# Kernel tuning notes

Measured on AMD Instinct MI355X. Metric: run time of the kernel, lower is better.

Reference implementation:

```python
import jax, jax.numpy as jnp
import numpy as np

B, N, D_IN, D_OUT = 2, 4096, 768, 768


def setup_inputs() -> dict:
    key = jax.random.key(0)
    kx, kq, kk, kv = jax.random.split(key, 4)
    x = jax.random.normal(kx, (B, N, D_IN), dtype=jnp.float32)
    # Linear(d_in, d_out, bias=False) weights, stored as [d_in, d_out]
    scale = 1.0 / np.sqrt(D_IN)
    Wq = jax.random.normal(kq, (D_IN, D_OUT), dtype=jnp.float32) * scale
    Wk = jax.random.normal(kk, (D_IN, D_OUT), dtype=jnp.float32) * scale
    Wv = jax.random.normal(kv, (D_IN, D_OUT), dtype=jnp.float32) * scale
    return {"x": x, "Wq": Wq, "Wk": Wk, "Wv": Wv}


def reference(x, Wq, Wk, Wv):
    # q,k,v: [B, N, D_OUT]
    q = jnp.einsum('bnd,de->bne', x, Wq)
    k = jnp.einsum('bnd,de->bne', x, Wk)
    v = jnp.einsum('bnd,de->bne', x, Wv)
    # Full [B, N, N] score matrix (naive attention, as in source).
    # NOTE: source's masked_fill is non-in-place and discarded, so NO causal
    # mask is actually applied -- reproduced faithfully here.
    scores = jnp.einsum('bqe,bke->bqk', q, k) / jnp.sqrt(jnp.float32(k.shape[-1]))
    weights = jax.nn.softmax(scores, axis=-1)
    # dropout rate 0.0 / eval mode -> identity
    out = jnp.einsum('bqk,bke->bqe', weights, v)  # [B, N, D_OUT]
    return out
```

## Files before the change

kernel.cpp:

```cpp
#include <hip/hip_runtime.h>

typedef __bf16 bf16x8 __attribute__((ext_vector_type(8)));
typedef float f32x4 __attribute__((ext_vector_type(4)));
typedef unsigned short us8 __attribute__((ext_vector_type(8)));

#define GAS __attribute__((address_space(1)))
#define LAS __attribute__((address_space(3)))

__device__ __forceinline__ unsigned short f32_to_bf16(float f) {
    unsigned int u = __float_as_uint(f);
    u += 0x7FFFu + ((u >> 16) & 1u);
    return (unsigned short)(u >> 16);
}

__device__ __forceinline__ float bf16_to_f32(unsigned short h) {
    return __uint_as_float((unsigned int)h << 16);
}

__device__ __forceinline__ void load16(const unsigned short* g, unsigned short* l) {
    __builtin_amdgcn_global_load_lds((GAS unsigned int*)g, (LAS unsigned int*)l, 16, 0, 0);
}

__global__ __launch_bounds__(1024) void prep(
    const float* __restrict__ x, unsigned short* __restrict__ Xbf,
    const float* __restrict__ W0, const float* __restrict__ W1, const float* __restrict__ W2,
    unsigned short* __restrict__ T0, unsigned short* __restrict__ T1, unsigned short* __restrict__ T2)
{
    __shared__ float tile[32][33];
    const int id = blockIdx.x;
    const int t = threadIdx.x;
    if (id < 1536) {
        int i = id * 1024 + t;
        float4 v = ((const float4*)x)[i];
        ushort4 o;
        o.x = f32_to_bf16(v.x); o.y = f32_to_bf16(v.y);
        o.z = f32_to_bf16(v.z); o.w = f32_to_bf16(v.w);
        ((ushort4*)Xbf)[i] = o;
    } else {
        const int tid = id - 1536;
        const int z = tid / 576, rem = tid % 576;
        const int by = rem / 24, bx = rem % 24;
        const float* W = (z == 0) ? W0 : (z == 1) ? W1 : W2;
        unsigned short* T = (z == 0) ? T0 : (z == 1) ? T1 : T2;
        const int r0 = by * 32, c0 = bx * 32;
        const int tx = t & 31, ty = t >> 5;
        tile[ty][tx] = W[(size_t)(r0 + ty) * 768 + c0 + tx];
        __syncthreads();
        T[(size_t)(c0 + ty) * 768 + r0 + tx] = f32_to_bf16(tile[tx][ty]);
    }
}

template <typename CT>
__global__ __launch_bounds__(256) void gemm_nt(
    const unsigned short* __restrict__ A, const unsigned short* __restrict__ B,
    CT* __restrict__ C, int K, int lda, int ldb, int ldc,
    size_t sA, size_t sB, size_t sC, float alpha)
{
    A += (size_t)blockIdx.z * sA;
    B += (size_t)blockIdx.z * sB;
    C += (size_t)blockIdx.z * sC;
    const int m0 = blockIdx.y * 128;
    const int n0 = blockIdx.x * 128;
    const int t = threadIdx.x;
    const int lane = t & 63;
    const int w = t >> 6;
    const int wm = (w >> 1) * 64;
    const int wn = (w & 1) * 64;

    __shared__ unsigned short At[128 * 64];
    __shared__ unsigned short Bt[128 * 64];

    f32x4 acc[4][4];
#pragma unroll
    for (int i = 0; i < 4; ++i)
#pragma unroll
        for (int j = 0; j < 4; ++j) acc[i][j] = (f32x4){0.f, 0.f, 0.f, 0.f};

    const int r15 = lane & 15;
    const int qa = lane >> 4;

    for (int k0 = 0; k0 < K; k0 += 64) {
#pragma unroll
        for (int i = 0; i < 4; ++i) {
            const int c = i * 256 + t;
            const int row = c >> 3;
            const int cc = (c & 7) ^ (row & 7);
            load16(A + (size_t)(m0 + row) * lda + k0 + cc * 8, &At[c * 8]);
            load16(B + (size_t)(n0 + row) * ldb + k0 + cc * 8, &Bt[c * 8]);
        }
        __syncthreads();

#pragma unroll
        for (int ks = 0; ks < 2; ++ks) {
            bf16x8 af[4], bf[4];
#pragma unroll
            for (int mi = 0; mi < 4; ++mi) {
                const int row = wm + mi * 16 + r15;
                af[mi] = *(const bf16x8*)&At[row * 64 + (((ks << 2) + qa) ^ (row & 7)) * 8];
            }
#pragma unroll
            for (int ni = 0; ni < 4; ++ni) {
                const int row = wn + ni * 16 + r15;
                bf[ni] = *(const bf16x8*)&Bt[row * 64 + (((ks << 2) + qa) ^ (row & 7)) * 8];
            }
#pragma unroll
            for (int mi = 0; mi < 4; ++mi)
#pragma unroll
                for (int ni = 0; ni < 4; ++ni)
                    acc[mi][ni] = __builtin_amdgcn_mfma_f32_16x16x32_bf16(
                        af[mi], bf[ni], acc[mi][ni], 0, 0, 0);
        }
        __syncthreads();
    }

    const int cr = (lane >> 4) * 4;
#pragma unroll
    for (int mi = 0; mi < 4; ++mi) {
#pragma unroll
        for (int ni = 0; ni < 4; ++ni) {
            const int gm = m0 + wm + mi * 16 + cr;
            const int gn = n0 + wn + ni * 16 + r15;
#pragma unroll
            for (int r = 0; r < 4; ++r) {
                float v = alpha * acc[mi][ni][r];
                if constexpr (sizeof(CT) == 2)
                    C[(size_t)(gm + r) * ldc + gn] = (CT)f32_to_bf16(v);
                else
                    C[(size_t)(gm + r) * ldc + gn] = v;
            }
        }
    }
}

template <int NT, bool EXP>
__device__ __forceinline__ void gemm256_core(
    const unsigned short* __restrict__ A, const unsigned short* __restrict__ B,
    unsigned short* __restrict__ C,
    int m0, int n0, int lda, int ldb, int ldc, float alpha)
{
    __shared__ unsigned short As[2][256 * 64];
    __shared__ unsigned short Bs[2][256 * 64];

    const int t = threadIdx.x;
    const int lane = t & 63;
    const int w = t >> 6;
    const int wm = (w >> 2) * 128;
    const int wn = (w & 3) * 64;
    const int r15 = lane & 15;
    const int qa = lane >> 4;

    const unsigned short* srcA[4];
    const unsigned short* srcB[4];
    int dstOff[4];
#pragma unroll
    for (int i = 0; i < 4; ++i) {
        const int c = i * 512 + t;
        const int row = c >> 3;
        const int cc = (c & 7) ^ (row & 7);
        srcA[i] = A + (size_t)(m0 + row) * lda + cc * 8;
        srcB[i] = B + (size_t)(n0 + row) * ldb + cc * 8;
        dstOff[i] = c * 8;
    }

    auto stageA = [&](int b, int kbase) {
#pragma unroll
        for (int i = 0; i < 4; ++i)
            load16(srcA[i] + kbase, &As[b][dstOff[i]]);
    };
    auto stageB = [&](int b, int kbase) {
#pragma unroll
        for (int i = 0; i < 4; ++i)
            load16(srcB[i] + kbase, &Bs[b][dstOff[i]]);
    };

    int offA[8][2], offB[4][2];
#pragma unroll
    for (int mi = 0; mi < 8; ++mi) {
        const int row = wm + mi * 16 + r15;
#pragma unroll
        for (int ks = 0; ks < 2; ++ks)
            offA[mi][ks] = row * 64 + (((ks << 2) + qa) ^ (row & 7)) * 8;
    }
#pragma unroll
    for (int ni = 0; ni < 4; ++ni) {
        const int row = wn + ni * 16 + r15;
#pragma unroll
        for (int ks = 0; ks < 2; ++ks)
            offB[ni][ks] = row * 64 + (((ks << 2) + qa) ^ (row & 7)) * 8;
    }

    f32x4 acc[8][4];
#pragma unroll
    for (int i = 0; i < 8; ++i)
#pragma unroll
        for (int j = 0; j < 4; ++j) acc[i][j] = (f32x4){0.f, 0.f, 0.f, 0.f};

    stageA(0, 0);
    stageB(0, 0);
    asm volatile("s_waitcnt vmcnt(0)" ::: "memory");
    __builtin_amdgcn_s_barrier();

    for (int tt = 0; tt < NT; ++tt) {
        const int b = tt & 1;
        const bool st = (tt + 1) < NT;
        const int kn = (tt + 1) << 6;

#pragma unroll
        for (int ks = 0; ks < 2; ++ks) {
            bf16x8 bB[4];
#pragma unroll
            for (int mh = 0; mh < 2; ++mh) {
                bf16x8 aA[4];
#pragma unroll
                for (int i = 0; i < 4; ++i)
                    aA[i] = *(const bf16x8*)&As[b][offA[mh * 4 + i][ks]];
                if (mh == 0) {
#pragma unroll
                    for (int ni = 0; ni < 4; ++ni)
                        bB[ni] = *(const bf16x8*)&Bs[b][offB[ni][ks]];
                }
                if (ks == 0 && mh == 0 && st) {
                    stageA(b ^ 1, kn);
                    stageB(b ^ 1, kn);
                }

                __builtin_amdgcn_s_barrier();
                asm volatile("s_waitcnt lgkmcnt(0)" ::: "memory");
                __builtin_amdgcn_s_setprio(1);
#pragma unroll
                for (int i = 0; i < 4; ++i)
#pragma unroll
                    for (int ni = 0; ni < 4; ++ni)
                        acc[mh * 4 + i][ni] = __builtin_amdgcn_mfma_f32_16x16x32_bf16(
                            aA[i], bB[ni], acc[mh * 4 + i][ni], 0, 0, 0);
                __builtin_amdgcn_s_setprio(0);
                if (ks == 1 && mh == 1) {
                    asm volatile("s_waitcnt vmcnt(0)" ::: "memory");
                    __builtin_amdgcn_s_barrier();
                } else {
                    __builtin_amdgcn_s_barrier();
                }
            }
        }
    }

    const int cr = (lane >> 4) * 4;
#pragma unroll
    for (int mi = 0; mi < 8; ++mi) {
#pragma unroll
        for (int ni = 0; ni < 4; ++ni) {
            const int gm = m0 + wm + mi * 16 + cr;
            const int gn = n0 + wn + ni * 16 + r15;
#pragma unroll
            for (int r = 0; r < 4; ++r) {
                float v = alpha * acc[mi][ni][r];
                if constexpr (EXP) v = __expf(v);
                C[(size_t)(gm + r) * ldc + gn] = f32_to_bf16(v);
            }
        }
    }
}

__global__ __launch_bounds__(512, 2) void gemm_s_exp2(
    const unsigned short* __restrict__ Q, const unsigned short* __restrict__ Kb,
    unsigned short* __restrict__ Sexp, float alpha)
{
    const unsigned short* A = Q + (size_t)blockIdx.z * 3145728;
    const unsigned short* B = Kb + (size_t)blockIdx.z * 3145728;
    unsigned short* C = Sexp + (size_t)blockIdx.z * 16777216;
    gemm256_core<12, true>(A, B, C, blockIdx.y * 256, blockIdx.x * 256,
                           768, 768, 4096, alpha);
}

__global__ __launch_bounds__(512, 2) void gemm_splitk2(
    const unsigned short* __restrict__ P, const unsigned short* __restrict__ Vt,
    unsigned short* __restrict__ Part)
{
    const int z = blockIdx.z;
    const int batch = z & 1;
    const int split = z >> 1;
    const unsigned short* A = P + (size_t)batch * 16777216 + (size_t)split * 2048;
    const unsigned short* B = Vt + (size_t)batch * 4096 + (size_t)split * 2048;
    unsigned short* C = Part + (size_t)z * 3145728;
    gemm256_core<32, false>(A, B, C, blockIdx.y * 256, blockIdx.x * 256,
                            4096, 8192, 768, 1.0f);
}

__global__ __launch_bounds__(256) void reduce_norm_rows(
    const unsigned short* __restrict__ Sexp, const unsigned short* __restrict__ Part,
    float* __restrict__ out)
{
    const int g = blockIdx.x;
    const int batch = g >> 12;
    const int r = g & 4095;
    const int t = threadIdx.x;
    const int wv = t >> 6, ln = t & 63;

    const unsigned short* srow = Sexp + (size_t)batch * 16777216 + (size_t)r * 4096;
    us8 a = ((const us8*)srow)[t];
    us8 b = ((const us8*)srow)[t + 256];
    float s = 0.f;
#pragma unroll
    for (int j = 0; j < 8; ++j) s += bf16_to_f32(a[j]) + bf16_to_f32(b[j]);
#pragma unroll
    for (int off = 32; off > 0; off >>= 1) s += __shfl_down(s, off, 64);
    __shared__ float red[4];
    if (ln == 0) red[wv] = s;
    __syncthreads();
    const float inv = 1.f / (red[0] + red[1] + red[2] + red[3]);

    if (t < 192) {
        const int c = t * 4;
        float4 acc = {0.f, 0.f, 0.f, 0.f};
#pragma unroll
        for (int sgroup = 0; sgroup < 2; ++sgroup) {
            const unsigned short* p = Part
                + ((size_t)(sgroup * 2 + batch) * 4096 + r) * 768 + c;
            ushort4 u = *(const ushort4*)p;
            acc.x += bf16_to_f32(u.x);
            acc.y += bf16_to_f32(u.y);
            acc.z += bf16_to_f32(u.z);
            acc.w += bf16_to_f32(u.w);
        }
        float4 o;
        o.x = acc.x * inv; o.y = acc.y * inv; o.z = acc.z * inv; o.w = acc.w * inv;
        *(float4*)(out + (size_t)g * 768 + c) = o;
    }
}

extern "C" void kernel_launch(void* const* d_in, const int* in_sizes, int n_in,
                              void* d_out, int out_size, void* d_ws, size_t ws_size,
                              hipStream_t stream) {
    const float* x  = (const float*)d_in[0];
    const float* Wq = (const float*)d_in[1];
    const float* Wk = (const float*)d_in[2];
    const float* Wv = (const float*)d_in[3];
    float* out = (float*)d_out;

    char* base = (char*)d_ws;
    size_t off = 0;
    auto alloc = [&](size_t b) { char* p = base + off; off += (b + 255) & ~(size_t)255; return p; };

    unsigned short* Xbf = (unsigned short*)alloc(8192ull * 768 * 2);
    unsigned short* WqT = (unsigned short*)alloc(768ull * 768 * 2);
    unsigned short* WkT = (unsigned short*)alloc(768ull * 768 * 2);
    unsigned short* WvT = (unsigned short*)alloc(768ull * 768 * 2);
    unsigned short* Qb  = (unsigned short*)alloc(8192ull * 768 * 2);
    unsigned short* Kb  = (unsigned short*)alloc(8192ull * 768 * 2);
    unsigned short* Vt  = (unsigned short*)alloc(768ull * 8192 * 2);
    unsigned short* Sexp = (unsigned short*)alloc(2ull * 4096 * 4096 * 2);
    unsigned short* Part = (unsigned short*)alloc(4ull * 3145728 * 2);
    (void)ws_size; (void)in_sizes; (void)n_in; (void)out_size; (void)WkT;

    prep<<<dim3(3264), dim3(1024), 0, stream>>>(x, Xbf, Wq, Wk, Wv, WqT, WkT, WvT);
    gemm_nt<unsigned short><<<dim3(6, 64, 2), dim3(256), 0, stream>>>(
        Xbf, WqT, Qb, 768, 768, 768, 768,
         0,  589824,  6291456, 1.0f);
    gemm_nt<unsigned short><<<dim3(64, 6, 1), dim3(256), 0, stream>>>(
        WvT, Xbf, Vt, 768, 768, 768, 8192, 0, 0, 0, 1.0f);
    gemm_s_exp2<<<dim3(16, 16, 2), dim3(512), 0, stream>>>(
        Qb, Kb, Sexp, 0.03608439182435161f);
    gemm_splitk2<<<dim3(3, 16, 4), dim3(512), 0, stream>>>(Sexp, Vt, Part);
    reduce_norm_rows<<<dim3(8192), dim3(256), 0, stream>>>(Sexp, Part, out);
}
```

Measured before the change: 275.9 us.

## Prefetch two K-tiles ahead, map blocks to XCDs, retile split-K GEMM to 256x192

The core GEMM now issues loads for the next two K-tiles up front and refills a buffer right after consuming it. It waits with partial vmcnt counts instead of draining all loads every iteration, so global-to-LDS copies overlap more compute. Both attention GEMMs use a 1D grid with an explicit block-to-XCD mapping so neighbouring tiles share an XCD's L2. The PV split-K GEMM switches to 256x192 tiles, giving 256 blocks instead of 192 to fill the CUs better. The hardcoded vmcnt values depend on load counts per stage and are fragile if the tile shape changes.

Result: no change. 270.5 us (-1.9%).

```diff
diff --git a/kernel.cpp b/kernel.cpp
--- a/kernel.cpp
+++ b/kernel.cpp
@@ -132,48 +132,55 @@
     }
 }
 
-template <int NT, bool EXP>
+template <int NT, int BN64, bool EXP>
 __device__ __forceinline__ void gemm256_core(
     const unsigned short* __restrict__ A, const unsigned short* __restrict__ B,
     unsigned short* __restrict__ C,
     int m0, int n0, int lda, int ldb, int ldc, float alpha)
 {
+    constexpr int BN = BN64 * 64;
     __shared__ unsigned short As[2][256 * 64];
-    __shared__ unsigned short Bs[2][256 * 64];
+    __shared__ unsigned short Bs[2][BN * 64];
 
     const int t = threadIdx.x;
     const int lane = t & 63;
     const int w = t >> 6;
     const int wm = (w >> 2) * 128;
-    const int wn = (w & 3) * 64;
+    const int wn = (w & 3) * (BN / 4);
     const int r15 = lane & 15;
     const int qa = lane >> 4;
 
     const unsigned short* srcA[4];
-    const unsigned short* srcB[4];
-    int dstOff[4];
+    int dstA[4];
 #pragma unroll
     for (int i = 0; i < 4; ++i) {
         const int c = i * 512 + t;
         const int row = c >> 3;
         const int cc = (c & 7) ^ (row & 7);
         srcA[i] = A + (size_t)(m0 + row) * lda + cc * 8;
+        dstA[i] = c * 8;
+    }
+    const unsigned short* srcB[BN64];
+    int dstB[BN64];
+#pragma unroll
+    for (int i = 0; i < BN64; ++i) {
+        const int c = i * 512 + t;
+        const int row = c >> 3;
+        const int cc = (c & 7) ^ (row & 7);
         srcB[i] = B + (size_t)(n0 + row) * ldb + cc * 8;
-        dstOff[i] = c * 8;
-    }
-
-    auto stageA = [&](int b, int kbase) {
+        dstB[i] = c * 8;
+    }
+
+    auto stage = [&](int buf, int kbase) {
 #pragma unroll
         for (int i = 0; i < 4; ++i)
-            load16(srcA[i] + kbase, &As[b][dstOff[i]]);
+            load16(srcA[i] + kbase, &As[buf][dstA[i]]);
+#pragma unroll
+        for (int i = 0; i < BN64; ++i)
+            load16(srcB[i] + kbase, &Bs[buf][dstB[i]]);
     };
-    auto stageB = [&](int b, int kbase) {
-#pragma unroll
-        for (int i = 0; i < 4; ++i)
-            load16(srcB[i] + kbase, &Bs[b][dstOff[i]]);
-    };
-
-    int offA[8][2], offB[4][2];
+
+    int offA[8][2], offB[BN64][2];
 #pragma unroll
     for (int mi = 0; mi < 8; ++mi) {
         const int row = wm + mi * 16 + r15;
@@ -182,32 +189,37 @@
             offA[mi][ks] = row * 64 + (((ks << 2) + qa) ^ (row & 7)) * 8;
     }
 #pragma unroll
-    for (int ni = 0; ni < 4; ++ni) {
+    for (int ni = 0; ni < BN64; ++ni) {
         const int row = wn + ni * 16 + r15;
 #pragma unroll
         for (int ks = 0; ks < 2; ++ks)
             offB[ni][ks] = row * 64 + (((ks << 2) + qa) ^ (row & 7)) * 8;
     }
 
-    f32x4 acc[8][4];
+    f32x4 acc[8][BN64];
 #pragma unroll
     for (int i = 0; i < 8; ++i)
 #pragma unroll
-        for (int j = 0; j < 4; ++j) acc[i][j] = (f32x4){0.f, 0.f, 0.f, 0.f};
-
-    stageA(0, 0);
-    stageB(0, 0);
-    asm volatile("s_waitcnt vmcnt(0)" ::: "memory");
-    __builtin_amdgcn_s_barrier();
+        for (int j = 0; j < BN64; ++j) acc[i][j] = (f32x4){0.f, 0.f, 0.f, 0.f};
+
+    stage(0, 0);
+    stage(1, 64);
 
     for (int tt = 0; tt < NT; ++tt) {
         const int b = tt & 1;
-        const bool st = (tt + 1) < NT;
-        const int kn = (tt + 1) << 6;
+
+        if (tt == NT - 1) {
+            asm volatile("s_waitcnt vmcnt(0)" ::: "memory");
+        } else if constexpr (BN64 == 4) {
+            asm volatile("s_waitcnt vmcnt(8)" ::: "memory");
+        } else {
+            asm volatile("s_waitcnt vmcnt(7)" ::: "memory");
+        }
+        __builtin_amdgcn_s_barrier();
 
 #pragma unroll
         for (int ks = 0; ks < 2; ++ks) {
-            bf16x8 bB[4];
+            bf16x8 bB[BN64];
 #pragma unroll
             for (int mh = 0; mh < 2; ++mh) {
                 bf16x8 aA[4];
@@ -216,12 +228,8 @@
                     aA[i] = *(const bf16x8*)&As[b][offA[mh * 4 + i][ks]];
                 if (mh == 0) {
 #pragma unroll
-                    for (int ni = 0; ni < 4; ++ni)
+                    for (int ni = 0; ni < BN64; ++ni)
                         bB[ni] = *(const bf16x8*)&Bs[b][offB[ni][ks]];
-                }
-                if (ks == 0 && mh == 0 && st) {
-                    stageA(b ^ 1, kn);
-                    stageB(b ^ 1, kn);
                 }
 
                 __builtin_amdgcn_s_barrier();
@@ -230,25 +238,22 @@
 #pragma unroll
                 for (int i = 0; i < 4; ++i)
 #pragma unroll
-                    for (int ni = 0; ni < 4; ++ni)
+                    for (int ni = 0; ni < BN64; ++ni)
                         acc[mh * 4 + i][ni] = __builtin_amdgcn_mfma_f32_16x16x32_bf16(
                             aA[i], bB[ni], acc[mh * 4 + i][ni], 0, 0, 0);
                 __builtin_amdgcn_s_setprio(0);
-                if (ks == 1 && mh == 1) {
-                    asm volatile("s_waitcnt vmcnt(0)" ::: "memory");
-                    __builtin_amdgcn_s_barrier();
-                } else {
-                    __builtin_amdgcn_s_barrier();
-                }
-            }
-        }
+                __builtin_amdgcn_s_barrier();
+            }
+        }
+
+        if (tt + 2 < NT) stage(b, (tt + 2) << 6);
     }
 
     const int cr = (lane >> 4) * 4;
 #pragma unroll
     for (int mi = 0; mi < 8; ++mi) {
 #pragma unroll
-        for (int ni = 0; ni < 4; ++ni) {
+        for (int ni = 0; ni < BN64; ++ni) {
             const int gm = m0 + wm + mi * 16 + cr;
             const int gn = n0 + wn + ni * 16 + r15;
 #pragma unroll
@@ -265,25 +270,34 @@
     const unsigned short* __restrict__ Q, const unsigned short* __restrict__ Kb,
     unsigned short* __restrict__ Sexp, float alpha)
 {
-    const unsigned short* A = Q + (size_t)blockIdx.z * 3145728;
-    const unsigned short* B = Kb + (size_t)blockIdx.z * 3145728;
-    unsigned short* C = Sexp + (size_t)blockIdx.z * 16777216;
-    gemm256_core<12, true>(A, B, C, blockIdx.y * 256, blockIdx.x * 256,
-                           768, 768, 4096, alpha);
+    const int f = blockIdx.x;
+    const int xcd = f & 7;
+    const int local = f >> 3;
+    const int x = (xcd & 1) * 8 + (local & 7);
+    const int y = ((xcd >> 1) & 1) * 8 + (local >> 3);
+    const int bb = xcd >> 2;
+    const unsigned short* A = Q + (size_t)bb * 3145728;
+    const unsigned short* B = Kb + (size_t)bb * 3145728;
+    unsigned short* C = Sexp + (size_t)bb * 16777216;
+    gemm256_core<12, 4, true>(A, B, C, y * 256, x * 256, 768, 768, 4096, alpha);
 }
 
 __global__ __launch_bounds__(512, 2) void gemm_splitk2(
     const unsigned short* __restrict__ P, const unsigned short* __restrict__ Vt,
     unsigned short* __restrict__ Part)
 {
-    const int z = blockIdx.z;
+    const int f = blockIdx.x;
+    const int xcd = f & 7;
+    const int local = f >> 3;
+    const int j = local & 3;
+    const int y = (xcd & 1) * 8 + (local >> 2);
+    const int z = xcd >> 1;
     const int batch = z & 1;
     const int split = z >> 1;
     const unsigned short* A = P + (size_t)batch * 16777216 + (size_t)split * 2048;
     const unsigned short* B = Vt + (size_t)batch * 4096 + (size_t)split * 2048;
     unsigned short* C = Part + (size_t)z * 3145728;
-    gemm256_core<32, false>(A, B, C, blockIdx.y * 256, blockIdx.x * 256,
-                            4096, 8192, 768, 1.0f);
+    gemm256_core<32, 3, false>(A, B, C, y * 256, j * 192, 4096, 8192, 768, 1.0f);
 }
 
 __global__ __launch_bounds__(256) void reduce_norm_rows(
@@ -358,8 +372,8 @@
          0,  589824,  6291456, 1.0f);
     gemm_nt<unsigned short><<<dim3(64, 6, 1), dim3(256), 0, stream>>>(
         WvT, Xbf, Vt, 768, 768, 768, 8192, 0, 0, 0, 1.0f);
-    gemm_s_exp2<<<dim3(16, 16, 2), dim3(512), 0, stream>>>(
+    gemm_s_exp2<<<dim3(512), dim3(512), 0, stream>>>(
         Qb, Kb, Sexp, 0.03608439182435161f);
-    gemm_splitk2<<<dim3(3, 16, 4), dim3(512), 0, stream>>>(Sexp, Vt, Part);
+    gemm_splitk2<<<dim3(256), dim3(512), 0, stream>>>(Sexp, Vt, Part);
     reduce_norm_rows<<<dim3(8192), dim3(256), 0, stream>>>(Sexp, Part, out);
 }
```
